# Performance work log

Hardware: AMD Instinct MI355X
Metric: run time of the kernel (lower is better)

The kernel has to match this reference:

```python
import jax, jax.numpy as jnp
import numpy as np

L, B, H = 4096, 32, 512


def setup_inputs() -> dict:
    key = jax.random.key(0)
    k1, k2, k3, k4 = jax.random.split(key, 4)
    query = jax.random.normal(k1, (B, H), dtype=jnp.float32)
    key_val = jax.random.normal(k2, (L, B, H), dtype=jnp.float32)
    # torch Linear(2H, H, bias=False): weight is (H, 2H); we store transposed (2H, H)
    W = jax.random.normal(k3, (2 * H, H), dtype=jnp.float32) * (1.0 / np.sqrt(2 * H))
    v = jax.random.normal(k4, (H,), dtype=jnp.float32)
    return {"query": query, "key_val": key_val, "W": W, "v": v}


def reference(query, key_val, W, v):
    # concat([expand(query), key], -1) @ W == query @ W_q + key @ W_k
    Wq, Wk = W[:H], W[H:]                       # each (H, H)
    q_proj = query @ Wq                          # (B, H)
    k_proj = jnp.einsum('lbi,ih->lbh', key_val, Wk)  # (L, B, H)
    energy = jnp.tanh(q_proj[None, :, :] + k_proj)   # (L, B, H)
    scores = jnp.einsum('h,lbh->bl', v, energy)      # (B, L)
    return jax.nn.softmax(scores, axis=1)[:, None, :]  # (B, 1, L)
```

## Files before the change

kernel.cpp:

```cpp
#include <hip/hip_runtime.h>
#include <hip/hip_bf16.h>
#include <stdint.h>

#define L_DIM 4096
#define B_DIM 32
#define H_DIM 512
#define M_DIM (L_DIM * B_DIM)
#define K_DIM H_DIM

typedef _Float16 half8 __attribute__((ext_vector_type(8)));
typedef __fp16 fp16x2 __attribute__((ext_vector_type(2)));
typedef float floatx4 __attribute__((ext_vector_type(4)));

__device__ __forceinline__ float tanh_fast(float x) {
  float e = __builtin_amdgcn_exp2f(x * 2.88539008177793f);
  return 1.0f - 2.0f * __builtin_amdgcn_rcpf(e + 1.0f);
}

__device__ __forceinline__ uint2 pack4(const float4& f) {
  const fp16x2 p0 = __builtin_amdgcn_cvt_pkrtz(f.x, f.y);
  const fp16x2 p1 = __builtin_amdgcn_cvt_pkrtz(f.z, f.w);
  uint2 u;
  u.x = __builtin_bit_cast(unsigned, p0);
  u.y = __builtin_bit_cast(unsigned, p1);
  return u;
}

__global__ __launch_bounds__(512) void prep_kernel(const float* __restrict__ query,
                                                   const float* __restrict__ W,
                                                   float* __restrict__ qp,
                                                   _Float16* __restrict__ W2) {
  __shared__ float4 qred[512];
  if (blockIdx.x < 64) {
    const int t = blockIdx.x * 512 + threadIdx.x;
    const int l15 = t & 15;
    const int q = (t >> 4) & 3;
    const int nc = (t >> 6) & 31;
    const int kt = t >> 11;
    const int n = nc * 16 + l15;
    const int kbase = H_DIM + kt * 32 + q * 8;
    half8 h;
#pragma unroll
    for (int j = 0; j < 8; ++j)
      h[j] = (_Float16)W[(size_t)(kbase + j) * H_DIM + n];
    *(half8*)(W2 + (size_t)t * 8) = h;
  } else {
    const int b = blockIdx.x - 64;
    const int tid = threadIdx.x;
    const int hx = tid & 127;
    const int ky = tid >> 7;
    const int h = hx * 4;
    const float* qrow = query + b * H_DIM + ky * 128;
    const float* wrow = W + (size_t)(ky * 128) * H_DIM + h;
    float4 acc = make_float4(0.f, 0.f, 0.f, 0.f);
#pragma unroll 8
    for (int i = 0; i < 128; ++i) {
      const float qv = qrow[i];
      const float4 w4 = *(const float4*)(wrow + (size_t)i * H_DIM);
      acc.x += qv * w4.x; acc.y += qv * w4.y;
      acc.z += qv * w4.z; acc.w += qv * w4.w;
    }
    qred[tid] = acc;
    __syncthreads();
    if (ky == 0) {
      const float4 a1 = qred[tid + 128], a2 = qred[tid + 256], a3 = qred[tid + 384];
      acc.x += a1.x + a2.x + a3.x;
      acc.y += a1.y + a2.y + a3.y;
      acc.z += a1.z + a2.z + a3.z;
      acc.w += a1.w + a2.w + a3.w;
      *(float4*)(qp + (size_t)b * H_DIM + h) = acc;
    }
  }
}

__global__ __launch_bounds__(512, 4) void fused_gemm_kernel(
    const float* __restrict__ key, const _Float16* __restrict__ W2,
    const float* __restrict__ qp, const float* __restrict__ v,
    float* __restrict__ scores) {
  __shared__ __align__(16) _Float16 As[2][64 * 32];
  __shared__ float swave[8 * 64];

  const int tid = threadIdx.x;
  const int lane = tid & 63;
  const int wn = tid >> 6;
  const int l15 = lane & 15;
  const int quad = lane >> 4;
  const int m0 = blockIdx.x * 64;

  const int srow = tid >> 3;
  const int schunk = tid & 7;
  const float* ag = key + (size_t)(m0 + srow) * K_DIM + schunk * 4;
  const int adst = srow * 32 + schunk * 4;

  const half8* bptr = (const half8*)W2 + (size_t)(wn * 4) * 64 + lane;

  floatx4 acc[4][4];
#pragma unroll
  for (int fm = 0; fm < 4; ++fm)
#pragma unroll
    for (int fn = 0; fn < 4; ++fn) acc[fm][fn] = (floatx4)0.0f;

  float4 ra0 = *(const float4*)(ag);
  float4 rb[2];
  rb[1] = *(const float4*)(ag + 32);
  rb[0] = *(const float4*)(ag + 64);
  *(uint2*)(As[0] + adst) = pack4(ra0);
  asm volatile("s_waitcnt lgkmcnt(0)" ::: "memory");
  __builtin_amdgcn_s_barrier();
  __builtin_amdgcn_sched_barrier(0);

#pragma unroll
  for (int kt = 0; kt < 16; ++kt) {
    half8 bc[4];
#pragma unroll
    for (int fn = 0; fn < 4; ++fn) bc[fn] = bptr[fn * 64];
    bptr += 32 * 64;

    const _Float16* buf = As[kt & 1];
    half8 av[4];
#pragma unroll
    for (int fm = 0; fm < 4; ++fm)
      av[fm] = *(const half8*)(buf + (fm * 16 + l15) * 32 + quad * 8);

    if (kt < 15) {
      *(uint2*)(As[(kt + 1) & 1] + adst) = pack4(rb[(kt + 1) & 1]);
      if (kt < 13) rb[(kt + 1) & 1] = *(const float4*)(ag + (kt + 3) * 32);
    }

#pragma unroll
    for (int fm = 0; fm < 4; ++fm)
#pragma unroll
      for (int fn = 0; fn < 4; ++fn)
        acc[fm][fn] = __builtin_amdgcn_mfma_f32_16x16x32_f16(av[fm], bc[fn],
                                                             acc[fm][fn], 0, 0, 0);

    __builtin_amdgcn_sched_barrier(0);
    asm volatile("s_waitcnt lgkmcnt(0)" ::: "memory");
    __builtin_amdgcn_s_barrier();
    __builtin_amdgcn_sched_barrier(0);
  }

  float vv[4];
#pragma unroll
  for (int fn = 0; fn < 4; ++fn) vv[fn] = v[wn * 64 + fn * 16 + l15];

#pragma unroll
  for (int fm = 0; fm < 4; ++fm) {
#pragma unroll
    for (int r = 0; r < 4; ++r) {
      const int mrow = fm * 16 + quad * 4 + r;
      const float* qrow = qp + (size_t)(mrow & 31) * H_DIM;
      float rs = 0.f;
#pragma unroll
      for (int fn = 0; fn < 4; ++fn) {
        const int n = wn * 64 + fn * 16 + l15;
        const float x = qrow[n] + acc[fm][fn][r];
        rs += vv[fn] * tanh_fast(x);
      }
      rs += __shfl_xor(rs, 1);
      rs += __shfl_xor(rs, 2);
      rs += __shfl_xor(rs, 4);
      rs += __shfl_xor(rs, 8);
      if (l15 == 0) swave[wn * 64 + mrow] = rs;
    }
  }
  __syncthreads();
  if (tid < 64) {
    float s = 0.f;
#pragma unroll
    for (int j = 0; j < 8; ++j) s += swave[j * 64 + tid];
    const int m = m0 + tid;
    scores[(size_t)(m & 31) * L_DIM + (m >> 5)] = s;
  }
}

__global__ __launch_bounds__(256) void softmax_kernel(const float* __restrict__ scores,
                                                      float* __restrict__ out) {
  const int b = blockIdx.x;
  const int t = threadIdx.x;
  const int lane = t & 63;
  const int w = t >> 6;
  __shared__ float redm[4], reds[4];
  const float* srow = scores + (size_t)b * L_DIM;
  float s[16];
#pragma unroll
  for (int i = 0; i < 16; ++i) s[i] = srow[t + i * 256];
  float mx = s[0];
#pragma unroll
  for (int i = 1; i < 16; ++i) mx = fmaxf(mx, s[i]);
#pragma unroll
  for (int off = 1; off < 64; off <<= 1) mx = fmaxf(mx, __shfl_xor(mx, off));
  if (lane == 0) redm[w] = mx;
  __syncthreads();
  mx = fmaxf(fmaxf(redm[0], redm[1]), fmaxf(redm[2], redm[3]));
  float sum = 0.f;
#pragma unroll
  for (int i = 0; i < 16; ++i) {
    s[i] = __builtin_amdgcn_exp2f((s[i] - mx) * 1.44269504f);
    sum += s[i];
  }
#pragma unroll
  for (int off = 1; off < 64; off <<= 1) sum += __shfl_xor(sum, off);
  if (lane == 0) reds[w] = sum;
  __syncthreads();
  const float inv = 1.0f / (reds[0] + reds[1] + reds[2] + reds[3]);
#pragma unroll
  for (int i = 0; i < 16; ++i) out[(size_t)b * L_DIM + t + i * 256] = s[i] * inv;
}

extern "C" void kernel_launch(void* const* d_in, const int* in_sizes, int n_in,
                              void* d_out, int out_size, void* d_ws, size_t ws_size,
                              hipStream_t stream) {
  const float* query = (const float*)d_in[0];
  const float* key   = (const float*)d_in[1];
  const float* W     = (const float*)d_in[2];
  const float* v     = (const float*)d_in[3];
  float* out = (float*)d_out;

  char* ws = (char*)d_ws;
  float* qp       = (float*)ws;
  float* scores   = (float*)(ws + 65536);
  _Float16* W2    = (_Float16*)(ws + 65536 + 524288);

  prep_kernel<<<96, 512, 0, stream>>>(query, W, qp, W2);
  fused_gemm_kernel<<<M_DIM / 64, 512, 0, stream>>>(key, W2, qp, v, scores);
  softmax_kernel<<<B_DIM, 256, 0, stream>>>(scores, out);
}
```

Measured before the change: 422.2 us.

## Load A fragments directly to registers and stream W into LDS asynchronously

Restructures the fused GEMM so each wave owns a 32x128 output tile (2x8 MFMA fragments) instead of 64x64. The key activations are loaded straight from global memory into registers in MFMA fragment layout and converted to fp16 there, skipping the LDS staging for A. The W operand is instead streamed into double-buffered LDS with global_load_lds and waited on through vmcnt. This trades fewer LDS writes for A and more reuse of B fragments against a 64KB LDS footprint, which may reduce occupancy below the launch_bounds target.

```diff
diff --git a/kernel.cpp b/kernel.cpp
--- a/kernel.cpp
+++ b/kernel.cpp
@@ -24,6 +24,19 @@
   u.x = __builtin_bit_cast(unsigned, p0);
   u.y = __builtin_bit_cast(unsigned, p1);
   return u;
+}
+
+__device__ __forceinline__ half8 packfrag(const float4& lo, const float4& hi) {
+  const uint2 u0 = pack4(lo);
+  const uint2 u1 = pack4(hi);
+  const uint4 uu = make_uint4(u0.x, u0.y, u1.x, u1.y);
+  return __builtin_bit_cast(half8, uu);
+}
+
+__device__ __forceinline__ void gload_lds16(const void* g, void* l) {
+  __builtin_amdgcn_global_load_lds(
+      (const __attribute__((address_space(1))) void*)g,
+      (__attribute__((address_space(3))) void*)l, 16, 0, 0);
 }
 
 __global__ __launch_bounds__(512) void prep_kernel(const float* __restrict__ query,
@@ -77,83 +90,112 @@
     const float* __restrict__ key, const _Float16* __restrict__ W2,
     const float* __restrict__ qp, const float* __restrict__ v,
     float* __restrict__ scores) {
-  __shared__ __align__(16) _Float16 As[2][64 * 32];
-  __shared__ float swave[8 * 64];
+  __shared__ __align__(16) char Bs[2 * 32768];
+  __shared__ float swave[4 * 64];
 
   const int tid = threadIdx.x;
   const int lane = tid & 63;
   const int wn = tid >> 6;
+  const int wr = wn >> 2;
+  const int wc = wn & 3;
   const int l15 = lane & 15;
   const int quad = lane >> 4;
   const int m0 = blockIdx.x * 64;
 
-  const int srow = tid >> 3;
-  const int schunk = tid & 7;
-  const float* ag = key + (size_t)(m0 + srow) * K_DIM + schunk * 4;
-  const int adst = srow * 32 + schunk * 4;
-
-  const half8* bptr = (const half8*)W2 + (size_t)(wn * 4) * 64 + lane;
-
-  floatx4 acc[4][4];
-#pragma unroll
-  for (int fm = 0; fm < 4; ++fm)
-#pragma unroll
-    for (int fn = 0; fn < 4; ++fn) acc[fm][fn] = (floatx4)0.0f;
-
-  float4 ra0 = *(const float4*)(ag);
-  float4 rb[2];
-  rb[1] = *(const float4*)(ag + 32);
-  rb[0] = *(const float4*)(ag + 64);
-  *(uint2*)(As[0] + adst) = pack4(ra0);
-  asm volatile("s_waitcnt lgkmcnt(0)" ::: "memory");
-  __builtin_amdgcn_s_barrier();
-  __builtin_amdgcn_sched_barrier(0);
+  const float* agA = key + (size_t)(m0 + wr * 32 + l15) * K_DIM + quad * 8;
+  const float* agB = agA + (size_t)16 * K_DIM;
+
+  const char* wsrc = (const char*)W2 + (size_t)tid * 16;
+  char* wdst = Bs + wn * 1024;
+  const char* rbase = Bs + wc * 8192 + quad * 256 + l15 * 16;
+
+  floatx4 acc[2][8];
+#pragma unroll
+  for (int fm = 0; fm < 2; ++fm)
+#pragma unroll
+    for (int fn = 0; fn < 8; ++fn) acc[fm][fn] = (floatx4)0.0f;
+
+  float4 cA0 = *(const float4*)(agA);
+  float4 cA1 = *(const float4*)(agA + 4);
+  float4 cB0 = *(const float4*)(agB);
+  float4 cB1 = *(const float4*)(agB + 4);
+#pragma unroll
+  for (int i = 0; i < 4; ++i)
+    gload_lds16(wsrc + i * 8192, wdst + i * 8192);
 
 #pragma unroll
   for (int kt = 0; kt < 16; ++kt) {
-    half8 bc[4];
-#pragma unroll
-    for (int fn = 0; fn < 4; ++fn) bc[fn] = bptr[fn * 64];
-    bptr += 32 * 64;
-
-    const _Float16* buf = As[kt & 1];
-    half8 av[4];
-#pragma unroll
-    for (int fm = 0; fm < 4; ++fm)
-      av[fm] = *(const half8*)(buf + (fm * 16 + l15) * 32 + quad * 8);
-
+    float4 nA0, nA1, nB0, nB1;
     if (kt < 15) {
-      *(uint2*)(As[(kt + 1) & 1] + adst) = pack4(rb[(kt + 1) & 1]);
-      if (kt < 13) rb[(kt + 1) & 1] = *(const float4*)(ag + (kt + 3) * 32);
-    }
-
-#pragma unroll
-    for (int fm = 0; fm < 4; ++fm)
-#pragma unroll
-      for (int fn = 0; fn < 4; ++fn)
-        acc[fm][fn] = __builtin_amdgcn_mfma_f32_16x16x32_f16(av[fm], bc[fn],
-                                                             acc[fm][fn], 0, 0, 0);
-
+      nA0 = *(const float4*)(agA + (kt + 1) * 32);
+      nA1 = *(const float4*)(agA + (kt + 1) * 32 + 4);
+      nB0 = *(const float4*)(agB + (kt + 1) * 32);
+      nB1 = *(const float4*)(agB + (kt + 1) * 32 + 4);
+    }
     __builtin_amdgcn_sched_barrier(0);
-    asm volatile("s_waitcnt lgkmcnt(0)" ::: "memory");
+    if (kt < 15) asm volatile("s_waitcnt vmcnt(4)" ::: "memory");
+    else         asm volatile("s_waitcnt vmcnt(0)" ::: "memory");
+    __builtin_amdgcn_sched_barrier(0);
     __builtin_amdgcn_s_barrier();
     __builtin_amdgcn_sched_barrier(0);
-  }
-
-  float vv[4];
-#pragma unroll
-  for (int fn = 0; fn < 4; ++fn) vv[fn] = v[wn * 64 + fn * 16 + l15];
-
-#pragma unroll
-  for (int fm = 0; fm < 4; ++fm) {
+
+    if (kt < 15) {
+      const char* s = wsrc + (size_t)(kt + 1) * 32768;
+      char* d = wdst + ((kt + 1) & 1) * 32768;
+#pragma unroll
+      for (int i = 0; i < 4; ++i)
+        gload_lds16(s + i * 8192, d + i * 8192);
+    }
+
+    const half8 avA = packfrag(cA0, cA1);
+    const half8 avB = packfrag(cB0, cB1);
+
+    const char* rb = rbase + (kt & 1) * 32768;
+    {
+      const half8 b0 = *(const half8*)(rb + 0 * 1024);
+      const half8 b1 = *(const half8*)(rb + 1 * 1024);
+      const half8 b2 = *(const half8*)(rb + 2 * 1024);
+      const half8 b3 = *(const half8*)(rb + 3 * 1024);
+      acc[0][0] = __builtin_amdgcn_mfma_f32_16x16x32_f16(avA, b0, acc[0][0], 0, 0, 0);
+      acc[0][1] = __builtin_amdgcn_mfma_f32_16x16x32_f16(avA, b1, acc[0][1], 0, 0, 0);
+      acc[0][2] = __builtin_amdgcn_mfma_f32_16x16x32_f16(avA, b2, acc[0][2], 0, 0, 0);
+      acc[0][3] = __builtin_amdgcn_mfma_f32_16x16x32_f16(avA, b3, acc[0][3], 0, 0, 0);
+      acc[1][0] = __builtin_amdgcn_mfma_f32_16x16x32_f16(avB, b0, acc[1][0], 0, 0, 0);
+      acc[1][1] = __builtin_amdgcn_mfma_f32_16x16x32_f16(avB, b1, acc[1][1], 0, 0, 0);
+      acc[1][2] = __builtin_amdgcn_mfma_f32_16x16x32_f16(avB, b2, acc[1][2], 0, 0, 0);
+      acc[1][3] = __builtin_amdgcn_mfma_f32_16x16x32_f16(avB, b3, acc[1][3], 0, 0, 0);
+    }
+    {
+      const half8 b4 = *(const half8*)(rb + 4 * 1024);
+      const half8 b5 = *(const half8*)(rb + 5 * 1024);
+      const half8 b6 = *(const half8*)(rb + 6 * 1024);
+      const half8 b7 = *(const half8*)(rb + 7 * 1024);
+      acc[0][4] = __builtin_amdgcn_mfma_f32_16x16x32_f16(avA, b4, acc[0][4], 0, 0, 0);
+      acc[0][5] = __builtin_amdgcn_mfma_f32_16x16x32_f16(avA, b5, acc[0][5], 0, 0, 0);
+      acc[0][6] = __builtin_amdgcn_mfma_f32_16x16x32_f16(avA, b6, acc[0][6], 0, 0, 0);
+      acc[0][7] = __builtin_amdgcn_mfma_f32_16x16x32_f16(avA, b7, acc[0][7], 0, 0, 0);
+      acc[1][4] = __builtin_amdgcn_mfma_f32_16x16x32_f16(avB, b4, acc[1][4], 0, 0, 0);
+      acc[1][5] = __builtin_amdgcn_mfma_f32_16x16x32_f16(avB, b5, acc[1][5], 0, 0, 0);
+      acc[1][6] = __builtin_amdgcn_mfma_f32_16x16x32_f16(avB, b6, acc[1][6], 0, 0, 0);
+      acc[1][7] = __builtin_amdgcn_mfma_f32_16x16x32_f16(avB, b7, acc[1][7], 0, 0, 0);
+    }
+    cA0 = nA0; cA1 = nA1; cB0 = nB0; cB1 = nB1;
+  }
+
+  float vv[8];
+#pragma unroll
+  for (int fn = 0; fn < 8; ++fn) vv[fn] = v[wc * 128 + fn * 16 + l15];
+
+#pragma unroll
+  for (int fm = 0; fm < 2; ++fm) {
 #pragma unroll
     for (int r = 0; r < 4; ++r) {
-      const int mrow = fm * 16 + quad * 4 + r;
-      const float* qrow = qp + (size_t)(mrow & 31) * H_DIM;
+      const int mrow = wr * 32 + fm * 16 + quad * 4 + r;
+      const float* qrow = qp + (size_t)((m0 + mrow) & 31) * H_DIM;
       float rs = 0.f;
 #pragma unroll
-      for (int fn = 0; fn < 4; ++fn) {
-        const int n = wn * 64 + fn * 16 + l15;
+      for (int fn = 0; fn < 8; ++fn) {
+        const int n = wc * 128 + fn * 16 + l15;
         const float x = qrow[n] + acc[fm][fn][r];
         rs += vv[fn] * tanh_fast(x);
       }
@@ -161,14 +203,12 @@
       rs += __shfl_xor(rs, 2);
       rs += __shfl_xor(rs, 4);
       rs += __shfl_xor(rs, 8);
-      if (l15 == 0) swave[wn * 64 + mrow] = rs;
+      if (l15 == 0) swave[wc * 64 + mrow] = rs;
     }
   }
   __syncthreads();
   if (tid < 64) {
-    float s = 0.f;
-#pragma unroll
-    for (int j = 0; j < 8; ++j) s += swave[j * 64 + tid];
+    const float s = swave[tid] + swave[64 + tid] + swave[128 + tid] + swave[192 + tid];
     const int m = m0 + tid;
     scores[(size_t)(m & 31) * L_DIM + (m >> 5)] = s;
   }
```

Measured after the change: 491.4 us. 16.4% more time.
